# Kernel optimization log

Measured on AMD Instinct MI355X. Metric: run time of the kernel, lower is better.

## Reference

```python
import jax, jax.numpy as jnp
import numpy as np

N = 50000      # nodes per graph
E = 800000     # edges per graph
F_IN = 128     # num_node_features
HID = 128      # hidden_dim
OUT = 128      # output_dim
C = 40         # num_classes
NEG_SLOPE = 0.2


def setup_inputs() -> dict:
    key = jax.random.key(0)
    ks = jax.random.split(key, 28)
    def p(k, shape, scale=0.05):
        return jax.random.normal(k, shape, jnp.float32) * scale
    inp = {
        "x": jax.random.normal(ks[0], (N, F_IN), jnp.float32),
        "y": jax.random.normal(ks[1], (N, F_IN), jnp.float32),
        "edge_index_x": jax.random.randint(ks[2], (2, E), 0, N),
        "edge_index_y": jax.random.randint(ks[3], (2, E), 0, N),
        # MultiheadAttention 1 (packed qkv in_proj like torch)
        "attn1_in_w": p(ks[4], (3 * F_IN, F_IN)),
        "attn1_in_b": p(ks[5], (3 * F_IN,)),
        "attn1_out_w": p(ks[6], (F_IN, F_IN)),
        "attn1_out_b": p(ks[7], (F_IN,)),
        # MultiheadAttention 2
        "attn2_in_w": p(ks[8], (3 * F_IN, F_IN)),
        "attn2_in_b": p(ks[9], (3 * F_IN,)),
        "attn2_out_w": p(ks[10], (F_IN, F_IN)),
        "attn2_out_b": p(ks[11], (F_IN,)),
        # gat1 (shared by x and y paths)
        "gat1_w": p(ks[12], (HID, F_IN)),
        "gat1_asrc": p(ks[13], (HID,)),
        "gat1_adst": p(ks[14], (HID,)),
        "gat1_b": p(ks[15], (HID,)),
        # gat2_x
        "gat2x_w": p(ks[16], (OUT, HID)),
        "gat2x_asrc": p(ks[17], (OUT,)),
        "gat2x_adst": p(ks[18], (OUT,)),
        "gat2x_b": p(ks[19], (OUT,)),
        # gat2_y
        "gat2y_w": p(ks[20], (OUT, HID)),
        "gat2y_asrc": p(ks[21], (OUT,)),
        "gat2y_adst": p(ks[22], (OUT,)),
        "gat2y_b": p(ks[23], (OUT,)),
        # fc
        "fc_w": p(ks[24], (C, 2 * OUT + F_IN)),
        "fc_b": p(ks[25], (C,)),
    }
    return inp


def _mha_len1(x, in_w, in_b, out_w, out_b):
    # x.unsqueeze(0) in torch -> seq_len=1 (batch=N). Softmax over a single
    # key is identically 1, so attention output == V; q/k projections cancel.
    d = x.shape[-1]
    v = x @ in_w[2 * d:].T + in_b[2 * d:]
    return v @ out_w.T + out_b


def _gat_conv(x, edge_index, W, a_src, a_dst, b):
    # PyG GATConv, heads=1, concat=True, add_self_loops=True
    n = x.shape[0]
    loop = jnp.arange(n)
    src = jnp.concatenate([edge_index[0], loop])  # message sources j
    dst = jnp.concatenate([edge_index[1], loop])  # message targets i
    h = x @ W.T                                   # [n, out]
    e = jax.nn.leaky_relu((h @ a_src)[src] + (h @ a_dst)[dst], NEG_SLOPE)
    # segment softmax over destination node neighborhoods
    m = jax.ops.segment_max(e, dst, num_segments=n)
    ex = jnp.exp(e - m[dst])
    s = jax.ops.segment_sum(ex, dst, num_segments=n)
    alpha = ex / (s[dst] + 1e-16)
    out = jax.ops.segment_sum(alpha[:, None] * h[src], dst, num_segments=n)
    return out + b


def reference(x, y, edge_index_x, edge_index_y,
              attn1_in_w, attn1_in_b, attn1_out_w, attn1_out_b,
              attn2_in_w, attn2_in_b, attn2_out_w, attn2_out_b,
              gat1_w, gat1_asrc, gat1_adst, gat1_b,
              gat2x_w, gat2x_asrc, gat2x_adst, gat2x_b,
              gat2y_w, gat2y_asrc, gat2y_adst, gat2y_b,
              fc_w, fc_b):
    x_res = x
    xa = _mha_len1(x, attn1_in_w, attn1_in_b, attn1_out_w, attn1_out_b)
    hx = jax.nn.relu(_gat_conv(xa, edge_index_x, gat1_w, gat1_asrc, gat1_adst, gat1_b))
    # dropout is a no-op in eval mode
    ox = _gat_conv(hx, edge_index_x, gat2x_w, gat2x_asrc, gat2x_adst, gat2x_b)

    ya = _mha_len1(y, attn2_in_w, attn2_in_b, attn2_out_w, attn2_out_b)
    hy = jax.nn.relu(_gat_conv(ya, edge_index_y, gat1_w, gat1_asrc, gat1_adst, gat1_b))
    oy = _gat_conv(hy, edge_index_y, gat2y_w, gat2y_asrc, gat2y_adst, gat2y_b)

    fusion = jnp.concatenate([ox, oy, x_res], axis=1)
    out = fusion @ fc_w.T + fc_b
    return jax.nn.log_softmax(out, axis=1)
```

## Files before the change

kernel.cpp:

```cpp
#include <hip/hip_runtime.h>
#include <hip/hip_bf16.h>
#include <hip/hip_fp16.h>

#define NEG_SLOPE 0.2f
#define LOG_R 10
#define RPB (1 << LOG_R)
#define EPB 4096
#define CAPB 24576

typedef __attribute__((ext_vector_type(4))) float f32x4;
typedef __attribute__((ext_vector_type(2))) float f32x2;
typedef __attribute__((ext_vector_type(8))) short s16x8;

static __device__ __forceinline__ unsigned pkbf(float a, float b) {
    unsigned ua = __float_as_uint(a);
    ua = (ua + 0x7FFFu + ((ua >> 16) & 1u)) >> 16;
    unsigned ub = __float_as_uint(b);
    ub = (ub + 0x7FFFu + ((ub >> 16) & 1u)) & 0xFFFF0000u;
    return (ua & 0xFFFFu) | ub;
}
static __device__ __forceinline__ unsigned short bf1(float a) {
    unsigned ua = __float_as_uint(a);
    return (unsigned short)((ua + 0x7FFFu + ((ua >> 16) & 1u)) >> 16);
}
static __device__ __forceinline__ float bflo(unsigned u) { return __uint_as_float(u << 16); }
static __device__ __forceinline__ float bfhi(unsigned u) { return __uint_as_float(u & 0xFFFF0000u); }

__global__ __launch_bounds__(256) void mha_combine2(
    const float* __restrict__ iw1, const float* __restrict__ ib1,
    const float* __restrict__ ow1, const float* __restrict__ ob1,
    const float* __restrict__ iw2, const float* __restrict__ ib2,
    const float* __restrict__ ow2, const float* __restrict__ ob2,
    float* __restrict__ cw1, float* __restrict__ cb1,
    float* __restrict__ cw2, float* __restrict__ cb2)
{
    int idx = blockIdx.x * blockDim.x + threadIdx.x;
    int set = idx >> 14;
    int local = idx & 16383;
    int o = local >> 7, i = local & 127;
    const float* in_w  = set ? iw2 : iw1;
    const float* in_b  = set ? ib2 : ib1;
    const float* out_w = set ? ow2 : ow1;
    const float* out_b = set ? ob2 : ob1;
    float* combW = set ? cw2 : cw1;
    float* combb = set ? cb2 : cb1;
    float a = 0.f;
    for (int k = 0; k < 128; ++k)
        a = fmaf(out_w[o * 128 + k], in_w[(256 + k) * 128 + i], a);
    combW[local] = a;
    if (i == 0) {
        float b = out_b[o];
        for (int k = 0; k < 128; ++k)
            b = fmaf(out_w[o * 128 + k], in_b[256 + k], b);
        combb[o] = b;
    }
}

__global__ __launch_bounds__(256) void fcw_prep(
    const float* __restrict__ fcw, unsigned* __restrict__ wbf)
{
    int i = blockIdx.x * 256 + threadIdx.x;
    if (i >= 48 * 192) return;
    unsigned v = 0;
    if (i < 40 * 192) {
        float2 f = ((const float2*)fcw)[i];
        v = pkbf(f.x, f.y);
    }
    wbf[i] = v;
}

template<bool ABF, bool HFP8>
__global__ __launch_bounds__(256) void gemm_mfma2(
    const void* __restrict__ A0, const void* __restrict__ A1,
    const float* __restrict__ W0, const float* __restrict__ W1,
    const float* __restrict__ bias0, const float* __restrict__ bias1,
    const float* __restrict__ as0, const float* __restrict__ ad0,
    const float* __restrict__ as1, const float* __restrict__ ad1,
    void* __restrict__ h0, void* __restrict__ h1,
    float* __restrict__ ss0, float* __restrict__ sd0,
    float* __restrict__ ss1, float* __restrict__ sd1,
    unsigned* __restrict__ ao0, unsigned* __restrict__ ao1,
    int n, int half)
{
    __shared__ unsigned xl[64 * 64];
    __shared__ unsigned wl[128 * 64];

    int b = blockIdx.x;
    const void* Ain; const float *W, *bias, *asrc, *adst;
    void* hbs; float *ssrc, *sdst; unsigned* aout;
    if (b < half) { Ain = A0; W = W0; bias = bias0; asrc = as0; adst = ad0; hbs = h0; ssrc = ss0; sdst = sd0; aout = ao0; }
    else { b -= half; Ain = A1; W = W1; bias = bias1; asrc = as1; adst = ad1; hbs = h1; ssrc = ss1; sdst = sd1; aout = ao1; }

    const int t = threadIdx.x;
    const int row0 = b * 64;

#pragma unroll
    for (int i = 0; i < 4; ++i) {
        int q = t + i * 256;
        int r = q >> 4, sl = q & 15;
        int gr = row0 + r; if (gr >= n) gr = n - 1;
        unsigned p0, p1, p2, p3;
        if (ABF) {
            uint4 v = ((const uint4*)Ain)[(size_t)gr * 16 + sl];
            p0 = v.x; p1 = v.y; p2 = v.z; p3 = v.w;
        } else {
            float4 a = ((const float4*)Ain)[(size_t)gr * 32 + sl * 2];
            float4 bb = ((const float4*)Ain)[(size_t)gr * 32 + sl * 2 + 1];
            p0 = pkbf(a.x, a.y); p1 = pkbf(a.z, a.w);
            p2 = pkbf(bb.x, bb.y); p3 = pkbf(bb.z, bb.w);
            if (aout) ((uint4*)aout)[(size_t)gr * 16 + sl] = make_uint4(p0, p1, p2, p3);
        }
        int dsl = sl ^ (r & 7);
        *(uint4*)&xl[r * 64 + dsl * 4] = make_uint4(p0, p1, p2, p3);
    }
#pragma unroll
    for (int i = 0; i < 8; ++i) {
        int q = t + i * 256;
        int r = q >> 4, sl = q & 15;
        float4 a = ((const float4*)W)[(size_t)r * 32 + sl * 2];
        float4 bb = ((const float4*)W)[(size_t)r * 32 + sl * 2 + 1];
        int dsl = sl ^ (r & 7);
        *(uint4*)&wl[r * 64 + dsl * 4] = make_uint4(
            pkbf(a.x, a.y), pkbf(a.z, a.w), pkbf(bb.x, bb.y), pkbf(bb.z, bb.w));
    }
    __syncthreads();

    const int l = t & 63, w = t >> 6;
    const int c = l & 15, q4 = l >> 4;
    const int rloc = w * 16 + c;
    f32x4 acc[8];
#pragma unroll
    for (int nt = 0; nt < 8; ++nt) acc[nt] = (f32x4){0.f, 0.f, 0.f, 0.f};

#pragma unroll
    for (int s = 0; s < 4; ++s) {
        int slot = (s * 4 + q4) ^ (c & 7);
        s16x8 af = *(const s16x8*)&xl[rloc * 64 + slot * 4];
#pragma unroll
        for (int nt = 0; nt < 8; ++nt) {
            int wr = nt * 16 + c;
            s16x8 bfr = *(const s16x8*)&wl[wr * 64 + slot * 4];
            acc[nt] = __builtin_amdgcn_mfma_f32_16x16x32_bf16(af, bfr, acc[nt], 0, 0, 0);
        }
    }

    float bv[8], as8[8], ad8[8];
#pragma unroll
    for (int nt = 0; nt < 8; ++nt) {
        bv[nt]  = bias ? bias[nt * 16 + c] : 0.f;
        as8[nt] = asrc ? asrc[nt * 16 + c] : 0.f;
        ad8[nt] = asrc ? adst[nt * 16 + c] : 0.f;
    }
    float ps[4] = {0.f, 0.f, 0.f, 0.f}, pd[4] = {0.f, 0.f, 0.f, 0.f};
    const int grow0 = row0 + w * 16 + q4 * 4;
#pragma unroll
    for (int nt = 0; nt < 8; ++nt) {
#pragma unroll
        for (int j = 0; j < 4; ++j) {
            float val = acc[nt][j] + bv[nt];
            if (grow0 + j < n) {
                if (HFP8) {
                    unsigned b8 = (unsigned)__builtin_amdgcn_cvt_pk_fp8_f32(val, val, 0, false);
                    ((unsigned char*)hbs)[(size_t)(grow0 + j) * 128 + nt * 16 + c] = (unsigned char)b8;
                } else {
                    ((unsigned short*)hbs)[(size_t)(grow0 + j) * 128 + nt * 16 + c] = bf1(val);
                }
            }
            ps[j] = fmaf(val, as8[nt], ps[j]);
            pd[j] = fmaf(val, ad8[nt], pd[j]);
        }
    }
    if (asrc) {
#pragma unroll
        for (int j = 0; j < 4; ++j) {
            float a = ps[j], bb = pd[j];
#pragma unroll
            for (int o = 1; o < 16; o <<= 1) {
                a += __shfl_xor(a, o);
                bb += __shfl_xor(bb, o);
            }
            if (c == 0 && grow0 + j < n) { ssrc[grow0 + j] = a; sdst[grow0 + j] = bb; }
        }
    }
}


__global__ __launch_bounds__(256) void hist_bucket2(
    const int* __restrict__ eix, const int* __restrict__ eiy, int E, int n,
    int* __restrict__ bcx, int* __restrict__ bcy, int half)
{
    __shared__ int lh[64];
    int gb = blockIdx.x;
    const int* ei = eix; int* bc = bcx;
    if (gb >= half) { gb -= half; ei = eiy; bc = bcy; }
    int t = threadIdx.x;
    int ET = E + n;
    int nbk = (n + RPB - 1) >> LOG_R;
    for (int i = t; i < nbk; i += 256) lh[i] = 0;
    __syncthreads();
    for (int e = gb * 256 + t; e < ET; e += half * 256) {
        int d = (e < E) ? ei[E + e] : (e - E);
        atomicAdd(&lh[d >> LOG_R], 1);
    }
    __syncthreads();
    if (t < nbk) atomicAdd(&bc[t], lh[t]);
}

__global__ void bscan(
    const int* __restrict__ bcx, const int* __restrict__ bcy, int nbk,
    int* __restrict__ bbx, int* __restrict__ bby,
    int* __restrict__ curx, int* __restrict__ cury,
    int* __restrict__ offx_n, int* __restrict__ offy_n)
{
    int w = threadIdx.x >> 6, lane = threadIdx.x & 63;
    if (w > 1) return;
    const int* bc = w ? bcy : bcx;
    int* bb  = w ? bby : bbx;
    int* cur = w ? cury : curx;
    int* offn = w ? offy_n : offx_n;
    int c = (lane < nbk) ? bc[lane] : 0;
    int v = c;
#pragma unroll
    for (int o = 1; o < 64; o <<= 1) {
        int u = __shfl_up(v, o);
        if (lane >= o) v += u;
    }
    int excl = v - c;
    if (lane < nbk) { bb[lane] = excl; cur[lane] = excl; }
    if (lane == 63) { bb[nbk] = v; *offn = v; }
}

__global__ __launch_bounds__(256) void bucket_pass(
    const int* __restrict__ eix, const int* __restrict__ eiy, int E, int n,
    int* __restrict__ curx, int* __restrict__ cury,
    unsigned* __restrict__ pkx, unsigned* __restrict__ pky, int half)
{
    __shared__ int lhist[64], lbase[64], gbase[64], lpos[64];
    __shared__ unsigned stg[EPB];
    __shared__ int gidx[EPB];
    int gb = blockIdx.x;
    const int* ei = eix; int* bcur = curx; unsigned* pk = pkx;
    if (gb >= half) { gb -= half; ei = eiy; bcur = cury; pk = pky; }
    const int t = threadIdx.x;
    const int ET = E + n;
    const int nbk = (n + RPB - 1) >> LOG_R;
    const int base = gb * EPB;

    for (int i = t; i < nbk; i += 256) lhist[i] = 0;
    __syncthreads();

    unsigned mypk[16];
    int myb[16];
#pragma unroll
    for (int k = 0; k < 16; ++k) {
        int e = base + k * 256 + t;
        if (e < ET) {
            int s, d;
            if (e < E) { s = ei[e]; d = ei[E + e]; }
            else       { s = e - E; d = e - E; }
            myb[k] = d >> LOG_R;
            mypk[k] = ((unsigned)s << LOG_R) | (unsigned)(d & (RPB - 1));
            atomicAdd(&lhist[myb[k]], 1);
        } else myb[k] = -1;
    }
    __syncthreads();

    if (t < 64) {
        int c = (t < nbk) ? lhist[t] : 0;
        int v = c;
#pragma unroll
        for (int o = 1; o < 64; o <<= 1) {
            int u = __shfl_up(v, o);
            if (t >= o) v += u;
        }
        int excl = v - c;
        if (t < nbk) {
            lbase[t] = excl;
            lpos[t] = excl;
            gbase[t] = c ? atomicAdd(&bcur[t], c) : 0;
        }
    }
    __syncthreads();

#pragma unroll
    for (int k = 0; k < 16; ++k) {
        if (myb[k] >= 0) {
            int p = atomicAdd(&lpos[myb[k]], 1);
            stg[p] = mypk[k];
            gidx[p] = gbase[myb[k]] + (p - lbase[myb[k]]);
        }
    }
    __syncthreads();

    int tot = lbase[nbk - 1] + lhist[nbk - 1];
    for (int i = t; i < tot; i += 256) pk[gidx[i]] = stg[i];
}

__global__ __launch_bounds__(256) void fine_sort(
    const unsigned* __restrict__ pkx, const unsigned* __restrict__ pky,
    const int* __restrict__ bbx, const int* __restrict__ bby,
    int* __restrict__ offx, int* __restrict__ offy,
    unsigned short* __restrict__ csx, unsigned short* __restrict__ csy,
    int n, int half)
{
    __shared__ int cur[RPB];
    __shared__ int ws[256];
    __shared__ unsigned short outs[CAPB];
    int gb = blockIdx.x;
    const unsigned* pk; const int* bb; int* off; unsigned short* cs;
    if (gb < half) { pk = pkx; bb = bbx; off = offx; cs = csx; }
    else { gb -= half; pk = pky; bb = bby; off = offy; cs = csy; }
    const int t = threadIdx.x;
    const int d0 = gb << LOG_R;
    const int nd = min(RPB, n - d0);
    const int base = bb[gb];
    const int sz = bb[gb + 1] - base;

    for (int i = t; i < RPB; i += 256) cur[i] = 0;
    __syncthreads();
    for (int i = t; i < sz; i += 256)
        atomicAdd(&cur[pk[base + i] & (RPB - 1)], 1);
    __syncthreads();

    int c0 = cur[t * 4], c1 = cur[t * 4 + 1], c2 = cur[t * 4 + 2], c3 = cur[t * 4 + 3];
    int s = c0 + c1 + c2 + c3;
    ws[t] = s; __syncthreads();
    for (int o = 1; o < 256; o <<= 1) {
        int a = (t >= o) ? ws[t - o] : 0;
        __syncthreads();
        ws[t] += a;
        __syncthreads();
    }
    int ex = ws[t] - s;
    int e0 = ex, e1 = ex + c0, e2 = e1 + c1, e3 = e2 + c2;
    cur[t * 4] = e0; cur[t * 4 + 1] = e1; cur[t * 4 + 2] = e2; cur[t * 4 + 3] = e3;
    int i0 = t * 4;
    if (i0     < nd) off[d0 + i0]     = base + e0;
    if (i0 + 1 < nd) off[d0 + i0 + 1] = base + e1;
    if (i0 + 2 < nd) off[d0 + i0 + 2] = base + e2;
    if (i0 + 3 < nd) off[d0 + i0 + 3] = base + e3;
    __syncthreads();

    if (sz <= CAPB) {
        for (int i = t; i < sz; i += 256) {
            unsigned p = pk[base + i];
            int pos = atomicAdd(&cur[p & (RPB - 1)], 1);
            outs[pos] = (unsigned short)(p >> LOG_R);
        }
        __syncthreads();
        for (int i = t; i < sz; i += 256) cs[base + i] = outs[i];
    } else {
        for (int i = t; i < sz; i += 256) {
            unsigned p = pk[base + i];
            int pos = atomicAdd(&cur[p & (RPB - 1)], 1);
            cs[base + pos] = (unsigned short)(p >> LOG_R);
        }
    }
}

__global__ __launch_bounds__(256) void gat_aggregate2(
    const int* __restrict__ off0, const unsigned short* __restrict__ cs0,
    const float* __restrict__ ss0, const float* __restrict__ sd0,
    const unsigned char* __restrict__ hb0, const float* __restrict__ bias0,
    unsigned* __restrict__ out0,
    const int* __restrict__ off1, const unsigned short* __restrict__ cs1,
    const float* __restrict__ ss1, const float* __restrict__ sd1,
    const unsigned char* __restrict__ hb1, const float* __restrict__ bias1,
    unsigned* __restrict__ out1,
    int n, int relu, int half)
{
    __shared__ uint2 stg[4][4][32];
    int b = blockIdx.x;
    const int *off; const unsigned short *csrc; const float *ssrc, *sdst, *bias;
    const unsigned char* hb; unsigned* outu;
    if (b < half) { off = off0; csrc = cs0; ssrc = ss0; sdst = sd0; hb = hb0; bias = bias0; outu = out0; }
    else { b -= half; off = off1; csrc = cs1; ssrc = ss1; sdst = sd1; hb = hb1; bias = bias1; outu = out1; }

    const int w = threadIdx.x >> 6;
    const int lane = threadIdx.x & 63;
    const int qw = lane >> 4;
    const int l16 = lane & 15;
    int node = b * 16 + w * 4 + qw;
    const int valid = node < n;
    if (node >= n) node = n - 1;
    const int p0 = off[node], p1 = off[node + 1];
    const int deg = p1 - p0;
    const float sd = sdst[node];

    unsigned s0 = 0, s1 = 0;
    float e0 = 0.f, e1 = 0.f;
    if (l16 < deg) {
        s0 = csrc[p0 + l16];
        float v = ssrc[s0] + sd;
        v = (v > 0.f) ? v : NEG_SLOPE * v;
        e0 = __expf(v);
    }
    if (l16 + 16 < deg) {
        s1 = csrc[p0 + 16 + l16];
        float v = ssrc[s1] + sd;
        v = (v > 0.f) ? v : NEG_SLOPE * v;
        e1 = __expf(v);
    }
    float ssum = e0 + e1;
    for (int p = p0 + 32 + l16; p < p1; p += 16) {
        int s = csrc[p];
        float v = ssrc[s] + sd;
        v = (v > 0.f) ? v : NEG_SLOPE * v;
        ssum += __expf(v);
    }
#pragma unroll
    for (int o = 8; o; o >>= 1) ssum += __shfl_xor(ssum, o);

    stg[w][qw][l16]      = make_uint2(s0 << 7, __float_as_uint(e0));
    stg[w][qw][l16 + 16] = make_uint2(s1 << 7, __float_as_uint(e1));

    const unsigned clo = (unsigned)l16 * 8u;
    float a0 = 0.f, a1 = 0.f, a2 = 0.f, a3 = 0.f;
    float a4 = 0.f, a5 = 0.f, a6 = 0.f, a7 = 0.f;

    int jcap = deg < 32 ? deg : 32;
    int j = 0;
    for (; j + 8 <= jcap; j += 8) {
        uint2 q[8];
#pragma unroll
        for (int k = 0; k < 8; ++k) q[k] = stg[w][qw][j + k];
        uint2 u[8];
#pragma unroll
        for (int k = 0; k < 8; ++k)
            u[k] = *(const uint2*)(hb + (size_t)(q[k].x | clo));
#pragma unroll
        for (int k = 0; k < 8; ++k) {
            float e = __uint_as_float(q[k].y);
            f32x2 f0 = __builtin_amdgcn_cvt_pk_f32_fp8((int)u[k].x, false);
            f32x2 f1 = __builtin_amdgcn_cvt_pk_f32_fp8((int)u[k].x, true);
            f32x2 f2 = __builtin_amdgcn_cvt_pk_f32_fp8((int)u[k].y, false);
            f32x2 f3 = __builtin_amdgcn_cvt_pk_f32_fp8((int)u[k].y, true);
            a0 = fmaf(e, f0[0], a0); a1 = fmaf(e, f0[1], a1);
            a2 = fmaf(e, f1[0], a2); a3 = fmaf(e, f1[1], a3);
            a4 = fmaf(e, f2[0], a4); a5 = fmaf(e, f2[1], a5);
            a6 = fmaf(e, f3[0], a6); a7 = fmaf(e, f3[1], a7);
        }
    }
    for (; j < jcap; ++j) {
        uint2 q = stg[w][qw][j];
        uint2 u = *(const uint2*)(hb + (size_t)(q.x | clo));
        float e = __uint_as_float(q.y);
        f32x2 f0 = __builtin_amdgcn_cvt_pk_f32_fp8((int)u.x, false);
        f32x2 f1 = __builtin_amdgcn_cvt_pk_f32_fp8((int)u.x, true);
        f32x2 f2 = __builtin_amdgcn_cvt_pk_f32_fp8((int)u.y, false);
        f32x2 f3 = __builtin_amdgcn_cvt_pk_f32_fp8((int)u.y, true);
        a0 = fmaf(e, f0[0], a0); a1 = fmaf(e, f0[1], a1);
        a2 = fmaf(e, f1[0], a2); a3 = fmaf(e, f1[1], a3);
        a4 = fmaf(e, f2[0], a4); a5 = fmaf(e, f2[1], a5);
        a6 = fmaf(e, f3[0], a6); a7 = fmaf(e, f3[1], a7);
    }
    for (int p = p0 + 32; p < p1; ++p) {
        int s = csrc[p];
        float v = ssrc[s] + sd;
        v = (v > 0.f) ? v : NEG_SLOPE * v;
        float e = __expf(v);
        uint2 u = *(const uint2*)(hb + (((size_t)s << 7) | clo));
        f32x2 f0 = __builtin_amdgcn_cvt_pk_f32_fp8((int)u.x, false);
        f32x2 f1 = __builtin_amdgcn_cvt_pk_f32_fp8((int)u.x, true);
        f32x2 f2 = __builtin_amdgcn_cvt_pk_f32_fp8((int)u.y, false);
        f32x2 f3 = __builtin_amdgcn_cvt_pk_f32_fp8((int)u.y, true);
        a0 = fmaf(e, f0[0], a0); a1 = fmaf(e, f0[1], a1);
        a2 = fmaf(e, f1[0], a2); a3 = fmaf(e, f1[1], a3);
        a4 = fmaf(e, f2[0], a4); a5 = fmaf(e, f2[1], a5);
        a6 = fmaf(e, f3[0], a6); a7 = fmaf(e, f3[1], a7);
    }

    float inv = 1.f / (ssum + 1e-16f);
    float4 bva = ((const float4*)bias)[l16 * 2];
    float4 bvb = ((const float4*)bias)[l16 * 2 + 1];
    float o0 = fmaf(a0, inv, bva.x);
    float o1 = fmaf(a1, inv, bva.y);
    float o2 = fmaf(a2, inv, bva.z);
    float o3 = fmaf(a3, inv, bva.w);
    float o4 = fmaf(a4, inv, bvb.x);
    float o5 = fmaf(a5, inv, bvb.y);
    float o6 = fmaf(a6, inv, bvb.z);
    float o7 = fmaf(a7, inv, bvb.w);
    if (relu) {
        o0 = fmaxf(o0, 0.f); o1 = fmaxf(o1, 0.f);
        o2 = fmaxf(o2, 0.f); o3 = fmaxf(o3, 0.f);
        o4 = fmaxf(o4, 0.f); o5 = fmaxf(o5, 0.f);
        o6 = fmaxf(o6, 0.f); o7 = fmaxf(o7, 0.f);
    }
    if (valid)
        ((uint4*)(outu + (size_t)node * 64))[l16] =
            make_uint4(pkbf(o0, o1), pkbf(o2, o3), pkbf(o4, o5), pkbf(o6, o7));
}

__global__ __launch_bounds__(64) void fc_logsoftmax(
    const unsigned* __restrict__ oxu, const unsigned* __restrict__ oyu,
    const unsigned* __restrict__ xbf,
    const unsigned* __restrict__ wbf, const float* __restrict__ fcb,
    float* __restrict__ out, int n)
{
    __shared__ unsigned xl[16 * 192];
    const int t = threadIdx.x;
    const int row0 = blockIdx.x * 16;

#pragma unroll
    for (int i = 0; i < 12; ++i) {
        int q = t + i * 64;
        int r = q / 48, sl = q % 48;
        int gr = row0 + r; if (gr >= n) gr = n - 1;
        const unsigned* S = (sl < 16) ? oxu : ((sl < 32) ? oyu : xbf);
        int slo = (sl < 16) ? sl : ((sl < 32) ? sl - 16 : sl - 32);
        uint4 v = ((const uint4*)S)[(size_t)gr * 16 + slo];
        int dsl = sl ^ (r & 7);
        *(uint4*)&xl[r * 192 + dsl * 4] = v;
    }
    __syncthreads();

    const int c = t & 15, q4 = t >> 4;
    f32x4 acc[3];
#pragma unroll
    for (int nt = 0; nt < 3; ++nt) acc[nt] = (f32x4){0.f, 0.f, 0.f, 0.f};

#pragma unroll
    for (int ks = 0; ks < 12; ++ks) {
        int gslot = ks * 4 + q4;
        int slot = gslot ^ (c & 7);
        s16x8 af = *(const s16x8*)&xl[c * 192 + slot * 4];
#pragma unroll
        for (int nt = 0; nt < 3; ++nt) {
            int wr = nt * 16 + c;
            s16x8 bfr = *(const s16x8*)&wbf[(size_t)wr * 192 + gslot * 4];
            acc[nt] = __builtin_amdgcn_mfma_f32_16x16x32_bf16(af, bfr, acc[nt], 0, 0, 0);
        }
    }

    float vb[3];
#pragma unroll
    for (int nt = 0; nt < 3; ++nt) {
        int col = nt * 16 + c;
        vb[nt] = (col < 40) ? fcb[col] : 0.f;
    }
    const int grow0 = row0 + q4 * 4;
#pragma unroll
    for (int j = 0; j < 4; ++j) {
        float v0 = acc[0][j] + vb[0];
        float v1 = acc[1][j] + vb[1];
        float v2 = (c < 8) ? (acc[2][j] + vb[2]) : -INFINITY;
        float m0 = fmaxf(fmaxf(v0, v1), v2);
#pragma unroll
        for (int o = 1; o < 16; o <<= 1) m0 = fmaxf(m0, __shfl_xor(m0, o));
        float s0 = __expf(v0 - m0) + __expf(v1 - m0) + ((c < 8) ? __expf(v2 - m0) : 0.f);
#pragma unroll
        for (int o = 1; o < 16; o <<= 1) s0 += __shfl_xor(s0, o);
        float lse = m0 + logf(s0);
        int grow = grow0 + j;
        if (grow < n) {
            out[(size_t)grow * 40 + c] = v0 - lse;
            out[(size_t)grow * 40 + 16 + c] = v1 - lse;
            if (c < 8) out[(size_t)grow * 40 + 32 + c] = v2 - lse;
        }
    }
}

extern "C" void kernel_launch(void* const* d_in, const int* in_sizes, int n_in,
                              void* d_out, int out_size, void* d_ws, size_t ws_size,
                              hipStream_t stream)
{
    const float* x    = (const float*)d_in[0];
    const float* y    = (const float*)d_in[1];
    const int*   eix  = (const int*)d_in[2];
    const int*   eiy  = (const int*)d_in[3];
    const float* a1iw = (const float*)d_in[4];
    const float* a1ib = (const float*)d_in[5];
    const float* a1ow = (const float*)d_in[6];
    const float* a1ob = (const float*)d_in[7];
    const float* a2iw = (const float*)d_in[8];
    const float* a2ib = (const float*)d_in[9];
    const float* a2ow = (const float*)d_in[10];
    const float* a2ob = (const float*)d_in[11];
    const float* g1w  = (const float*)d_in[12];
    const float* g1as = (const float*)d_in[13];
    const float* g1ad = (const float*)d_in[14];
    const float* g1b  = (const float*)d_in[15];
    const float* g2xw = (const float*)d_in[16];
    const float* g2xas= (const float*)d_in[17];
    const float* g2xad= (const float*)d_in[18];
    const float* g2xb = (const float*)d_in[19];
    const float* g2yw = (const float*)d_in[20];
    const float* g2yas= (const float*)d_in[21];
    const float* g2yad= (const float*)d_in[22];
    const float* g2yb = (const float*)d_in[23];
    const float* fcw  = (const float*)d_in[24];
    const float* fcb  = (const float*)d_in[25];
    float* outp = (float*)d_out;

    const int N = in_sizes[0] / 128;
    const int E = in_sizes[2] / 2;
    (void)n_in; (void)out_size; (void)ws_size;

    size_t NU = (size_t)N * 64;
    unsigned* u0 = (unsigned*)d_ws;
    unsigned* u1 = u0 + NU;
    unsigned* u2 = u1 + NU;
    unsigned* u3 = u2 + NU;
    unsigned* u4 = u3 + NU;
    float* ssx = (float*)(u4 + NU);
    float* sdx = ssx + N;
    float* ssy = sdx + N;
    float* sdy = ssy + N;
    float* cw1 = sdy + N;
    float* cb1 = cw1 + 128 * 128;
    float* cw2 = cb1 + 128;
    float* cb2 = cw2 + 128 * 128;
    const int Npad = (N + 4) & ~3;
    int* offx = (int*)(cb2 + 128);
    int* offy = offx + Npad;
    int* bbx  = offy + Npad;
    int* bby  = bbx + 128;
    int* bcx  = bby + 128;
    int* bcy  = bcx + 64;
    int* curx = bcy + 64;
    int* cury = curx + 64;
    unsigned* pkx = (unsigned*)(cury + 64);
    unsigned* pky = pkx + (E + N);
    unsigned short* csx = (unsigned short*)(pky + (E + N));
    unsigned short* csy = csx + (((E + N) + 1) & ~1);
    unsigned* wbf = (unsigned*)(csy + (((E + N) + 1) & ~1));

    const int ET = E + N;
    const int NBK = (N + RPB - 1) >> LOG_R;
    const int gG = (N + 63) / 64;
    const int gA = (N + 15) / 16;
    const int nAB = (ET + EPB - 1) / EPB;

    mha_combine2<<<128, 256, 0, stream>>>(a1iw, a1ib, a1ow, a1ob,
                                          a2iw, a2ib, a2ow, a2ob,
                                          cw1, cb1, cw2, cb2);
    fcw_prep<<<(48 * 192 + 255) / 256, 256, 0, stream>>>(fcw, wbf);

    hipMemsetAsync(bcx, 0, 128 * sizeof(int), stream);
    hist_bucket2<<<256, 256, 0, stream>>>(eix, eiy, E, N, bcx, bcy, 128);
    bscan<<<1, 128, 0, stream>>>(bcx, bcy, NBK, bbx, bby, curx, cury, offx + N, offy + N);
    bucket_pass<<<2 * nAB, 256, 0, stream>>>(eix, eiy, E, N, curx, cury, pkx, pky, nAB);
    fine_sort<<<2 * NBK, 256, 0, stream>>>(pkx, pky, bbx, bby, offx, offy, csx, csy, N, NBK);

    gemm_mfma2<false, false><<<2 * gG, 256, 0, stream>>>(
        x, y, cw1, cw2, cb1, cb2,
        nullptr, nullptr, nullptr, nullptr,
        u0, u2,
        nullptr, nullptr, nullptr, nullptr,
        u4, nullptr, N, gG);

    gemm_mfma2<true, true><<<2 * gG, 256, 0, stream>>>(
        u0, u2, g1w, g1w, nullptr, nullptr,
        g1as, g1ad, g1as, g1ad,
        u1, u3,
        ssx, sdx, ssy, sdy,
        nullptr, nullptr, N, gG);
    gat_aggregate2<<<2 * gA, 256, 0, stream>>>(
        offx, csx, ssx, sdx, (const unsigned char*)u1, g1b, u0,
        offy, csy, ssy, sdy, (const unsigned char*)u3, g1b, u2,
        N, 1, gA);

    gemm_mfma2<true, true><<<2 * gG, 256, 0, stream>>>(
        u0, u2, g2xw, g2yw, nullptr, nullptr,
        g2xas, g2xad, g2yas, g2yad,
        u1, u3,
        ssx, sdx, ssy, sdy,
        nullptr, nullptr, N, gG);
    gat_aggregate2<<<2 * gA, 256, 0, stream>>>(
        offx, csx, ssx, sdx, (const unsigned char*)u1, g2xb, u0,
        offy, csy, ssy, sdy, (const unsigned char*)u3, g2yb, u2,
        N, 0, gA);

    fc_logsoftmax<<<(N + 15) / 16, 64, 0, stream>>>(u0, u2, u4, wbf, fcb, outp, N);
}
```

Before: 232.6 us.

## Fold MHA value/out projection into gat1 weights, drop one GEMM pass

```diff
diff --git a/kernel.cpp b/kernel.cpp
--- a/kernel.cpp
+++ b/kernel.cpp
@@ -56,6 +56,34 @@
     }
 }
 
+__global__ __launch_bounds__(256) void wcomb2(
+    const float* __restrict__ g1w,
+    const float* __restrict__ cw1, const float* __restrict__ cb1,
+    const float* __restrict__ cw2, const float* __restrict__ cb2,
+    float* __restrict__ w1x, float* __restrict__ b1x,
+    float* __restrict__ w1y, float* __restrict__ b1y)
+{
+    int idx = blockIdx.x * blockDim.x + threadIdx.x;
+    if (idx >= 2 * 16384) return;
+    int set = idx >> 14;
+    int local = idx & 16383;
+    int o = local >> 7, i = local & 127;
+    const float* cw = set ? cw2 : cw1;
+    const float* cb = set ? cb2 : cb1;
+    float* wo = set ? w1y : w1x;
+    float* bo = set ? b1y : b1x;
+    float a = 0.f;
+    for (int k = 0; k < 128; ++k)
+        a = fmaf(g1w[o * 128 + k], cw[k * 128 + i], a);
+    wo[local] = a;
+    if (i == 0) {
+        float b = 0.f;
+        for (int k = 0; k < 128; ++k)
+            b = fmaf(g1w[o * 128 + k], cb[k], b);
+        bo[o] = b;
+    }
+}
+
 __global__ __launch_bounds__(256) void fcw_prep(
     const float* __restrict__ fcw, unsigned* __restrict__ wbf)
 {
@@ -369,7 +397,7 @@
     unsigned* __restrict__ out1,
     int n, int relu, int half)
 {
-    __shared__ uint2 stg[4][4][32];
+    __shared__ uint2 stg[4][4][34];
     int b = blockIdx.x;
     const int *off; const unsigned short *csrc; const float *ssrc, *sdst, *bias;
     const unsigned char* hb; unsigned* outu;
@@ -625,6 +653,10 @@
     unsigned short* csx = (unsigned short*)(pky + (E + N));
     unsigned short* csy = csx + (((E + N) + 1) & ~1);
     unsigned* wbf = (unsigned*)(csy + (((E + N) + 1) & ~1));
+    float* w1cx = (float*)(wbf + 48 * 192);
+    float* b1cx = w1cx + 16384;
+    float* w1cy = b1cx + 128;
+    float* b1cy = w1cy + 16384;
 
     const int ET = E + N;
     const int NBK = (N + RPB - 1) >> LOG_R;
@@ -635,6 +667,8 @@
     mha_combine2<<<128, 256, 0, stream>>>(a1iw, a1ib, a1ow, a1ob,
                                           a2iw, a2ib, a2ow, a2ob,
                                           cw1, cb1, cw2, cb2);
+    wcomb2<<<128, 256, 0, stream>>>(g1w, cw1, cb1, cw2, cb2,
+                                    w1cx, b1cx, w1cy, b1cy);
     fcw_prep<<<(48 * 192 + 255) / 256, 256, 0, stream>>>(fcw, wbf);
 
     hipMemsetAsync(bcx, 0, 128 * sizeof(int), stream);
@@ -643,19 +677,12 @@
     bucket_pass<<<2 * nAB, 256, 0, stream>>>(eix, eiy, E, N, curx, cury, pkx, pky, nAB);
     fine_sort<<<2 * NBK, 256, 0, stream>>>(pkx, pky, bbx, bby, offx, offy, csx, csy, N, NBK);
 
-    gemm_mfma2<false, false><<<2 * gG, 256, 0, stream>>>(
-        x, y, cw1, cw2, cb1, cb2,
-        nullptr, nullptr, nullptr, nullptr,
-        u0, u2,
-        nullptr, nullptr, nullptr, nullptr,
-        u4, nullptr, N, gG);
-
-    gemm_mfma2<true, true><<<2 * gG, 256, 0, stream>>>(
-        u0, u2, g1w, g1w, nullptr, nullptr,
+    gemm_mfma2<false, true><<<2 * gG, 256, 0, stream>>>(
+        x, y, w1cx, w1cy, b1cx, b1cy,
         g1as, g1ad, g1as, g1ad,
         u1, u3,
         ssx, sdx, ssy, sdy,
-        nullptr, nullptr, N, gG);
+        u4, nullptr, N, gG);
     gat_aggregate2<<<2 * gA, 256, 0, stream>>>(
         offx, csx, ssx, sdx, (const unsigned char*)u1, g1b, u0,
         offy, csy, ssy, sdy, (const unsigned char*)u3, g1b, u2,
```

Result: faster. 222.6 us (-4.3%).
